# Performance work log

Hardware: AMD Instinct MI355X
Metric: run time of the kernel (lower is better)

## Reference

```python
import jax, jax.numpy as jnp
import numpy as np

B, N, C = 256, 256, 128   # batch (=N_res rows), seq len, pair channels
H, D = 4, 128             # heads, per-head dim (== output_dim per module code)
O = 128                   # output_dim


def _glorot(key, shape, fan_in, fan_out):
    limit = np.sqrt(6.0 / (fan_in + fan_out))
    return jax.random.uniform(key, shape, jnp.float32, -limit, limit)


def setup_inputs() -> dict:
    key = jax.random.key(0)
    ks = jax.random.split(key, 9)
    q_data = jax.random.normal(ks[0], (B, N, C), jnp.float32)
    m_data = jax.random.normal(ks[1], (B, N, C), jnp.float32)
    bias = jax.random.normal(ks[2], (B, 1, N, N), jnp.float32)
    nonbatched_bias = jax.random.normal(ks[3], (H, N, N), jnp.float32)
    query_w = _glorot(ks[4], (C, H, D), C, H * D)
    key_w = _glorot(ks[5], (C, H, D), C, H * D)
    value_w = _glorot(ks[6], (C, H, D), C, H * D)
    gating_w = jnp.zeros((C, H, D), jnp.float32)
    gating_b = jnp.ones((H, D), jnp.float32)
    output_w = _glorot(ks[7], (H, D, O), H * D, O)
    output_b = jnp.zeros((O,), jnp.float32)
    return {
        'q_data': q_data, 'm_data': m_data, 'bias': bias,
        'nonbatched_bias': nonbatched_bias,
        'query_w': query_w, 'key_w': key_w, 'value_w': value_w,
        'gating_w': gating_w, 'gating_b': gating_b,
        'output_w': output_w, 'output_b': output_b,
    }


def reference(q_data, m_data, bias, nonbatched_bias,
              query_w, key_w, value_w, gating_w, gating_b,
              output_w, output_b):
    key_dim = query_w.shape[-1]  # per-head dim (tied to output_dim in module)
    q = jnp.einsum('bqa,ahc->bqhc', q_data, query_w) * key_dim ** (-0.5)
    k = jnp.einsum('bka,ahc->bkhc', m_data, key_w)
    v = jnp.einsum('bka,ahc->bkhc', m_data, value_w)
    logits = jnp.einsum('bqhc,bkhc->bhqk', q, k) + bias
    logits = logits + nonbatched_bias[None]  # broadcast shared bias over batch
    weights = jax.nn.softmax(logits, axis=-1)
    weighted_avg = jnp.einsum('bhqk,bkhc->bqhc', weights, v)
    gate = jax.nn.sigmoid(jnp.einsum('bqc,chv->bqhv', q_data, gating_w) + gating_b)
    weighted_avg = weighted_avg * gate
    return jnp.einsum('bqhc,hco->bqo', weighted_avg, output_w) + output_b
```

## Files before the change

kernel.cpp:

```cpp
#include <hip/hip_runtime.h>
#include <stdint.h>


typedef unsigned short u16;
typedef u16 u16x8 __attribute__((ext_vector_type(8)));
typedef u16 u16x4 __attribute__((ext_vector_type(4)));
typedef __bf16 bf16x8 __attribute__((ext_vector_type(8)));
typedef float floatx4 __attribute__((ext_vector_type(4)));

union B8 { u16x8 u; bf16x8 b; };

__device__ __forceinline__ float bf2f(u16 u) {
  union { uint32_t i; float f; } v; v.i = ((uint32_t)u) << 16; return v.f;
}
__device__ __forceinline__ u16 f2bf(float f) {
  union { float f; uint32_t i; } v; v.f = f;
  return (u16)((v.i + 0x7fffu + ((v.i >> 16) & 1u)) >> 16);
}
__device__ __forceinline__ bf16x8 ld8(const u16* p) { return *(const bf16x8*)p; }
__device__ __forceinline__ floatx4 mfma16(bf16x8 a, bf16x8 b, floatx4 c) {
  return __builtin_amdgcn_mfma_f32_16x16x32_bf16(a, b, c, 0, 0, 0);
}
__device__ __forceinline__ void cfence() { asm volatile("" ::: "memory"); }

template<bool BF>
__device__ __forceinline__ bf16x8 ldin8(const void* p, long long idx) {
  if constexpr (BF) {
    return *(const bf16x8*)((const u16*)p + idx);
  } else {
    const float* f = (const float*)p + idx;
    floatx4 a = *(const floatx4*)f;
    floatx4 b = *(const floatx4*)(f + 4);
    B8 r;
    #pragma unroll
    for (int i = 0; i < 4; ++i) { r.u[i] = f2bf(a[i]); r.u[i + 4] = f2bf(b[i]); }
    return r.b;
  }
}
template<bool BF>
__device__ __forceinline__ float ldin1(const void* p, long long idx) {
  if constexpr (BF) return bf2f(((const u16*)p)[idx]);
  else              return ((const float*)p)[idx];
}

template<bool BF>
__device__ __forceinline__ void pre_body(
    const void* qw, const void* kw, const void* vw, const void* gw,
    const void* ow, u16* wt)
{
  const int blk = blockIdx.x, tid = threadIdx.x;
  if (blk < 16) {
    const int mat = blk >> 2, h = blk & 3;
    const void* W = (mat == 0) ? qw : (mat == 1) ? kw : (mat == 2) ? vw : gw;
    u16* dst = wt + blk * 16384;
    for (int idx = tid; idx < 16384; idx += 256) {
      int c = idx >> 7, d = idx & 127;
      dst[d * 128 + c] = f2bf(ldin1<BF>(W, (long long)c * 512 + h * 128 + d));
    }
  } else {
    const int part = blk - 16;
    u16* dst = wt + 16 * 16384;
    for (int idx = tid; idx < 16384; idx += 256) {
      int k = idx >> 7, o = idx & 127;
      int kg = part * 128 + k;
      dst[o * 512 + kg] = f2bf(ldin1<BF>(ow, (long long)kg * 128 + o));
    }
  }
}

__global__ __launch_bounds__(256) void k_pre(
    const void* qw, const void* kw, const void* vw, const void* gw,
    const void* ow, const void* gating_b, u16* wt)
{
  const bool bf = (*(const uint32_t*)gating_b) == 0x3F803F80u;
  if (bf) pre_body<true >(qw, kw, vw, gw, ow, wt);
  else    pre_body<false>(qw, kw, vw, gw, ow, wt);
}

template<bool BF>
__device__ __forceinline__ void fused_body(
    const void* q_data, const void* m_data,
    const void* __restrict__ bias, const void* __restrict__ nbias,
    const void* gating_b, const u16* __restrict__ wt,
    u16* Ob, int b0, int Bc, u16* smem)
{
  const int tid  = threadIdx.x;
  const int lane = tid & 63, w = tid >> 6;
  const int quad = lane >> 4, l15 = lane & 15;
  const int l7   = l15 & 7;

  const int nwg = Bc * 4, id = blockIdx.x;
  const int xcd = id & 7, rest = id >> 3;
  const int qq = nwg >> 3, rm = nwg & 7;
  const int swz = (xcd < rm ? xcd * (qq + 1) : rm * (qq + 1) + (xcd - rm) * qq) + rest;
  const int bl = swz >> 2, h = swz & 3;
  const int bg = b0 + bl;
  const long long bh = (long long)(bl * 4 + h);

  u16* Kl  = smem;
  u16* Vtl = Kl + 32768;
  u16* sPw = Vtl + 32768 + w * 1152;

  const u16* wtQ = wt + (0 * 4 + h) * 16384;
  const u16* wtK = wt + (1 * 4 + h) * 16384;
  const u16* wtV = wt + (2 * 4 + h) * 16384;
  const u16* wtG = wt + (3 * 4 + h) * 16384;
  const float scale = 0.088388347648318447f;

  bf16x8 aq[2][4];
  u16* Qs = Kl + w * 4096;
  #pragma unroll
  for (int p = 0; p < 2; ++p) {
    const int m0 = p * 128 + w * 16;
    floatx4 qa[8];
    #pragma unroll
    for (int ni = 0; ni < 8; ++ni) qa[ni] = (floatx4){0.f, 0.f, 0.f, 0.f};
    #pragma unroll
    for (int ks = 0; ks < 4; ++ks) {
      bf16x8 aA = ldin8<BF>(q_data, ((long long)bg * 256 + m0 + l15) * 128 + ks * 32 + quad * 8);
      #pragma unroll
      for (int ni = 0; ni < 8; ++ni) {
        bf16x8 bw = ld8(wtQ + (ni * 16 + l15) * 128 + ks * 32 + quad * 8);
        qa[ni] = mfma16(aA, bw, qa[ni]);
      }
    }
    #pragma unroll
    for (int ni = 0; ni < 8; ++ni)
      #pragma unroll
      for (int r = 0; r < 4; ++r)
        Qs[(quad * 4 + r) * 136 + ni * 16 + l15] = f2bf(qa[ni][r] * scale);
    cfence();
    #pragma unroll
    for (int ks = 0; ks < 4; ++ks)
      aq[p][ks] = ld8(Qs + l15 * 136 + ks * 32 + quad * 8);
    cfence();
  }
  __syncthreads();

  const int nb = w * 32;
  {
    floatx4 ka[2][8];
    #pragma unroll
    for (int mi = 0; mi < 2; ++mi)
      #pragma unroll
      for (int ni = 0; ni < 8; ++ni) ka[mi][ni] = (floatx4){0.f, 0.f, 0.f, 0.f};
    #pragma unroll
    for (int ks = 0; ks < 4; ++ks) {
      bf16x8 bw[8];
      #pragma unroll
      for (int ni = 0; ni < 8; ++ni)
        bw[ni] = ld8(wtK + (ni * 16 + l15) * 128 + ks * 32 + quad * 8);
      #pragma unroll
      for (int mi = 0; mi < 2; ++mi) {
        bf16x8 aA = ldin8<BF>(m_data, ((long long)bg * 256 + nb + mi * 16 + l15) * 128 + ks * 32 + quad * 8);
        #pragma unroll
        for (int ni = 0; ni < 8; ++ni)
          ka[mi][ni] = mfma16(aA, bw[ni], ka[mi][ni]);
      }
    }
    #pragma unroll
    for (int mi = 0; mi < 2; ++mi)
      #pragma unroll
      for (int ni = 0; ni < 8; ++ni)
        #pragma unroll
        for (int r = 0; r < 4; ++r) {
          int n = nb + mi * 16 + quad * 4 + r;
          int d = ni * 16 + l15;
          Kl[n * 128 + (d ^ ((n & 7) << 3))] = f2bf(ka[mi][ni][r]);
        }
  }
  {
    floatx4 va[2][8];
    #pragma unroll
    for (int mi = 0; mi < 2; ++mi)
      #pragma unroll
      for (int ni = 0; ni < 8; ++ni) va[mi][ni] = (floatx4){0.f, 0.f, 0.f, 0.f};
    #pragma unroll
    for (int ks = 0; ks < 4; ++ks) {
      bf16x8 bw[8];
      #pragma unroll
      for (int ni = 0; ni < 8; ++ni)
        bw[ni] = ld8(wtV + (ni * 16 + l15) * 128 + ks * 32 + quad * 8);
      #pragma unroll
      for (int mi = 0; mi < 2; ++mi) {
        bf16x8 aA = ldin8<BF>(m_data, ((long long)bg * 256 + nb + mi * 16 + l15) * 128 + ks * 32 + quad * 8);
        #pragma unroll
        for (int ni = 0; ni < 8; ++ni)
          va[mi][ni] = mfma16(aA, bw[ni], va[mi][ni]);
      }
    }
    #pragma unroll
    for (int mi = 0; mi < 2; ++mi)
      #pragma unroll
      for (int ni = 0; ni < 8; ++ni) {
        int d = ni * 16 + l15;
        int n4 = nb + mi * 16 + quad * 4;
        u16x4 v4;
        #pragma unroll
        for (int r = 0; r < 4; ++r) v4[r] = f2bf(va[mi][ni][r]);
        *(u16x4*)(Vtl + d * 256 + (n4 ^ ((d & 7) << 3))) = v4;
      }
  }
  __syncthreads();

  #pragma unroll
  for (int p = 0; p < 2; ++p) {
    const int m0 = p * 128 + w * 16;

    floatx4 s[16];
    #pragma unroll
    for (int nt = 0; nt < 16; ++nt) s[nt] = (floatx4){0.f, 0.f, 0.f, 0.f};
    #pragma unroll
    for (int kc = 0; kc < 4; ++kc) {
      float bz[4][4];
      #pragma unroll
      for (int ntl = 0; ntl < 4; ++ntl)
        #pragma unroll
        for (int r = 0; r < 4; ++r) {
          long long gi = ((long long)bg * 256 + m0 + quad * 4 + r) * 256 + kc * 64 + ntl * 16 + l15;
          long long gn = ((long long)h * 256 + m0 + quad * 4 + r) * 256 + kc * 64 + ntl * 16 + l15;
          bz[ntl][r] = ldin1<BF>(bias, gi) + ldin1<BF>(nbias, gn);
        }
      #pragma unroll
      for (int ntl = 0; ntl < 4; ++ntl) {
        const int nt = kc * 4 + ntl;
        #pragma unroll
        for (int ks = 0; ks < 4; ++ks) {
          bf16x8 bk = ld8(Kl + (kc * 64 + ntl * 16 + l15) * 128 +
                          ((ks * 32 + quad * 8) ^ (l7 << 3)));
          s[nt] = mfma16(aq[p][ks], bk, s[nt]);
        }
        #pragma unroll
        for (int r = 0; r < 4; ++r) s[nt][r] += bz[ntl][r];
      }
    }

    float mx[4] = {-1e30f, -1e30f, -1e30f, -1e30f};
    #pragma unroll
    for (int nt = 0; nt < 16; ++nt)
      #pragma unroll
      for (int r = 0; r < 4; ++r) mx[r] = fmaxf(mx[r], s[nt][r]);
    #pragma unroll
    for (int r = 0; r < 4; ++r)
      #pragma unroll
      for (int off = 1; off < 16; off <<= 1)
        mx[r] = fmaxf(mx[r], __shfl_xor(mx[r], off));
    float sm[4] = {0.f, 0.f, 0.f, 0.f};
    #pragma unroll
    for (int nt = 0; nt < 16; ++nt)
      #pragma unroll
      for (int r = 0; r < 4; ++r) {
        float e = __expf(s[nt][r] - mx[r]);
        s[nt][r] = e; sm[r] += e;
      }
    #pragma unroll
    for (int r = 0; r < 4; ++r)
      #pragma unroll
      for (int off = 1; off < 16; off <<= 1)
        sm[r] += __shfl_xor(sm[r], off);
    float inv[4];
    #pragma unroll
    for (int r = 0; r < 4; ++r) inv[r] = 1.f / sm[r];

    floatx4 o[8];
    #pragma unroll
    for (int dt = 0; dt < 8; ++dt) o[dt] = (floatx4){0.f, 0.f, 0.f, 0.f};
    #pragma unroll
    for (int c = 0; c < 4; ++c) {
      #pragma unroll
      for (int ntl = 0; ntl < 4; ++ntl)
        #pragma unroll
        for (int r = 0; r < 4; ++r)
          sPw[(quad * 4 + r) * 72 + ntl * 16 + l15] = f2bf(s[c * 4 + ntl][r]);
      cfence();
      bf16x8 ap[2];
      #pragma unroll
      for (int k2 = 0; k2 < 2; ++k2)
        ap[k2] = ld8(sPw + l15 * 72 + k2 * 32 + quad * 8);
      #pragma unroll
      for (int dt = 0; dt < 8; ++dt)
        #pragma unroll
        for (int k2 = 0; k2 < 2; ++k2) {
          bf16x8 bv = ld8(Vtl + (dt * 16 + l15) * 256 +
                          ((c * 64 + k2 * 32 + quad * 8) ^ (l7 << 3)));
          o[dt] = mfma16(ap[k2], bv, o[dt]);
        }
      cfence();
    }

    bf16x8 aqd[4];
    #pragma unroll
    for (int ks = 0; ks < 4; ++ks)
      aqd[ks] = ldin8<BF>(q_data, ((long long)bg * 256 + m0 + l15) * 128 + ks * 32 + quad * 8);
    #pragma unroll
    for (int nt = 0; nt < 8; ++nt) {
      floatx4 g = (floatx4){0.f, 0.f, 0.f, 0.f};
      #pragma unroll
      for (int ks = 0; ks < 4; ++ks) {
        bf16x8 bw = ld8(wtG + (nt * 16 + l15) * 128 + ks * 32 + quad * 8);
        g = mfma16(aqd[ks], bw, g);
      }
      #pragma unroll
      for (int r = 0; r < 4; ++r) {
        int row = m0 + quad * 4 + r, d = nt * 16 + l15;
        float gate = 1.f / (1.f + __expf(-(g[r] + ldin1<BF>(gating_b, h * 128 + d))));
        Ob[(bh * 256 + row) * 128 + d] = f2bf(o[nt][r] * inv[r] * gate);
      }
    }
  }
}

__global__ __launch_bounds__(512, 2) void k_fused(
    const void* q_data, const void* m_data, const void* bias,
    const void* nbias, const void* gating_b, const u16* wt,
    u16* Ob, int b0, int Bc)
{
  __shared__ __align__(16) u16 smem[74752];
  const bool bf = (*(const uint32_t*)gating_b) == 0x3F803F80u;
  if (bf) fused_body<true >(q_data, m_data, bias, nbias, gating_b, wt, Ob, b0, Bc, smem);
  else    fused_body<false>(q_data, m_data, bias, nbias, gating_b, wt, Ob, b0, Bc, smem);
}

template<bool BF>
__device__ __forceinline__ void out_body(
    const u16* wsr, const u16* wtO, const void* output_b,
    void* out, int b0)
{
  const int tid  = threadIdx.x;
  const int lane = tid & 63, w = tid >> 6;
  const int quad = lane >> 4, l15 = lane & 15;
  const int wm = w >> 1, wn = w & 1;
  const int r0l = blockIdx.x * 32;
  const int bl  = r0l >> 8, n0 = r0l & 255;

  floatx4 acc[4];
  #pragma unroll
  for (int ni = 0; ni < 4; ++ni) acc[ni] = (floatx4){0.f, 0.f, 0.f, 0.f};

  #pragma unroll
  for (int kt = 0; kt < 4; ++kt) {
    #pragma unroll
    for (int ks = 0; ks < 4; ++ks) {
      bf16x8 af = ld8(wsr + ((long long)(bl * 4 + kt) * 256 + n0 + wm * 16 + l15) * 128
                          + ks * 32 + quad * 8);
      #pragma unroll
      for (int ni = 0; ni < 4; ++ni) {
        int col = wn * 64 + ni * 16 + l15;
        bf16x8 bw = ld8(wtO + (long long)col * 512 + kt * 128 + ks * 32 + quad * 8);
        acc[ni] = mfma16(af, bw, acc[ni]);
      }
    }
  }

  #pragma unroll
  for (int ni = 0; ni < 4; ++ni) {
    #pragma unroll
    for (int r = 0; r < 4; ++r) {
      int i = wm * 16 + quad * 4 + r;
      int j = wn * 64 + ni * 16 + l15;
      long long orow = (long long)b0 * 256 + r0l + i;
      float v = acc[ni][r] + ldin1<BF>(output_b, j);
      if constexpr (BF) ((u16*)out)[orow * 128 + j] = f2bf(v);
      else              ((float*)out)[orow * 128 + j] = v;
    }
  }
}

__global__ __launch_bounds__(256) void k_out(
    const u16* wsr, const u16* wtO, const void* output_b,
    const void* gating_b, void* out, int b0)
{
  const bool bf = (*(const uint32_t*)gating_b) == 0x3F803F80u;
  if (bf) out_body<true >(wsr, wtO, output_b, out, b0);
  else    out_body<false>(wsr, wtO, output_b, out, b0);
}

extern "C" void kernel_launch(void* const* d_in, const int* in_sizes, int n_in,
                              void* d_out, int out_size, void* d_ws, size_t ws_size,
                              hipStream_t stream)
{
  (void)in_sizes; (void)n_in; (void)out_size;
  const void* q_data   = d_in[0];
  const void* m_data   = d_in[1];
  const void* bias     = d_in[2];
  const void* nbias    = d_in[3];
  const void* query_w  = d_in[4];
  const void* key_w    = d_in[5];
  const void* value_w  = d_in[6];
  const void* gating_w = d_in[7];
  const void* gating_b = d_in[8];
  const void* output_w = d_in[9];
  const void* output_b = d_in[10];
  u16* ws = (u16*)d_ws;

  const long long wtElems = 16 * 16384 + 128 * 512;
  u16* wt  = ws;
  u16* wtO = wt + 16 * 16384;
  u16* reg = ws + wtElems;

  const size_t per_batch_bytes = 131072ull * 2;
  const size_t fixed_bytes = (size_t)wtElems * 2;
  int Bc = 1;
  while (Bc * 2 <= 256 &&
         fixed_bytes + (size_t)(Bc * 2) * per_batch_bytes <= ws_size) Bc *= 2;

  k_pre<<<20, 256, 0, stream>>>(query_w, key_w, value_w, gating_w,
                                output_w, gating_b, wt);

  for (int b0 = 0; b0 < 256; b0 += Bc) {
    k_fused<<<Bc * 4, 512, 0, stream>>>(q_data, m_data, bias, nbias,
                                        gating_b, wt, reg, b0, Bc);
    k_out<<<8 * Bc, 256, 0, stream>>>(reg, wtO, output_b,
                                      gating_b, d_out, b0);
  }
}
```

Before: 673.4 us.

## Use 1024-thread blocks with one 16-row query tile per wave, transposed score MFMA

Doubles the fused attention block to 16 waves so each wave handles a single 16-row query tile instead of looping over two. The score MFMA is transposed (K as the A operand), which lets bias and nonbatched bias be read as vectorized 4-wide loads and reduces softmax row reductions to two cross-lane shuffles. P is staged through a swizzled LDS buffer that reuses the K region after a barrier. The trade is fewer registers per thread, an extra block-wide sync, and likely one block per CU.

After: 625.1 us. 1.08x faster.

```diff
diff --git a/kernel.cpp b/kernel.cpp
--- a/kernel.cpp
+++ b/kernel.cpp
@@ -42,6 +42,18 @@
   if constexpr (BF) return bf2f(((const u16*)p)[idx]);
   else              return ((const float*)p)[idx];
 }
+template<bool BF>
+__device__ __forceinline__ floatx4 ldin4(const void* p, long long idx) {
+  floatx4 v;
+  if constexpr (BF) {
+    u16x4 u = *(const u16x4*)((const u16*)p + idx);
+    #pragma unroll
+    for (int i = 0; i < 4; ++i) v[i] = bf2f(u[i]);
+  } else {
+    v = *(const floatx4*)((const float*)p + idx);
+  }
+  return v;
+}
 
 template<bool BF>
 __device__ __forceinline__ void pre_body(
@@ -98,8 +110,7 @@
   const long long bh = (long long)(bl * 4 + h);
 
   u16* Kl  = smem;
-  u16* Vtl = Kl + 32768;
-  u16* sPw = Vtl + 32768 + w * 1152;
+  u16* Vtl = smem + 32768;
 
   const u16* wtQ = wt + (0 * 4 + h) * 16384;
   const u16* wtK = wt + (1 * 4 + h) * 16384;
@@ -107,11 +118,11 @@
   const u16* wtG = wt + (3 * 4 + h) * 16384;
   const float scale = 0.088388347648318447f;
 
-  bf16x8 aq[2][4];
-  u16* Qs = Kl + w * 4096;
-  #pragma unroll
-  for (int p = 0; p < 2; ++p) {
-    const int m0 = p * 128 + w * 16;
+  const int m0 = w * 16;
+
+  bf16x8 aq[4];
+  {
+    u16* Qs = (w < 8) ? (Kl + w * 2176) : (Vtl + (w - 8) * 2176);
     floatx4 qa[8];
     #pragma unroll
     for (int ni = 0; ni < 8; ++ni) qa[ni] = (floatx4){0.f, 0.f, 0.f, 0.f};
@@ -132,190 +143,156 @@
     cfence();
     #pragma unroll
     for (int ks = 0; ks < 4; ++ks)
-      aq[p][ks] = ld8(Qs + l15 * 136 + ks * 32 + quad * 8);
+      aq[ks] = ld8(Qs + l15 * 136 + ks * 32 + quad * 8);
+  }
+  __syncthreads();
+
+  {
+    bf16x8 aA[4];
+    #pragma unroll
+    for (int ks = 0; ks < 4; ++ks)
+      aA[ks] = ldin8<BF>(m_data, ((long long)bg * 256 + m0 + l15) * 128 + ks * 32 + quad * 8);
+
+    floatx4 ka[8];
+    #pragma unroll
+    for (int ni = 0; ni < 8; ++ni) ka[ni] = (floatx4){0.f, 0.f, 0.f, 0.f};
+    #pragma unroll
+    for (int ks = 0; ks < 4; ++ks)
+      #pragma unroll
+      for (int ni = 0; ni < 8; ++ni) {
+        bf16x8 bw = ld8(wtK + (ni * 16 + l15) * 128 + ks * 32 + quad * 8);
+        ka[ni] = mfma16(aA[ks], bw, ka[ni]);
+      }
+    #pragma unroll
+    for (int ni = 0; ni < 8; ++ni)
+      #pragma unroll
+      for (int r = 0; r < 4; ++r) {
+        int n = m0 + quad * 4 + r, d = ni * 16 + l15;
+        Kl[n * 128 + (d ^ ((n & 7) << 3))] = f2bf(ka[ni][r]);
+      }
+
+    floatx4 va[8];
+    #pragma unroll
+    for (int ni = 0; ni < 8; ++ni) va[ni] = (floatx4){0.f, 0.f, 0.f, 0.f};
+    #pragma unroll
+    for (int ks = 0; ks < 4; ++ks)
+      #pragma unroll
+      for (int ni = 0; ni < 8; ++ni) {
+        bf16x8 bw = ld8(wtV + (ni * 16 + l15) * 128 + ks * 32 + quad * 8);
+        va[ni] = mfma16(aA[ks], bw, va[ni]);
+      }
+    #pragma unroll
+    for (int ni = 0; ni < 8; ++ni) {
+      int d = ni * 16 + l15, n4 = m0 + quad * 4;
+      u16x4 vv;
+      #pragma unroll
+      for (int r = 0; r < 4; ++r) vv[r] = f2bf(va[ni][r]);
+      *(u16x4*)(Vtl + d * 256 + (n4 ^ ((d & 7) << 3))) = vv;
+    }
+  }
+  __syncthreads();
+
+  floatx4 s[16];
+  #pragma unroll
+  for (int nt = 0; nt < 16; ++nt) {
+    long long gi = ((long long)bg * 256 + m0 + l15) * 256 + nt * 16 + quad * 4;
+    long long gn = ((long long)h  * 256 + m0 + l15) * 256 + nt * 16 + quad * 4;
+    floatx4 bv = ldin4<BF>(bias, gi);
+    floatx4 nv = ldin4<BF>(nbias, gn);
+    #pragma unroll
+    for (int r = 0; r < 4; ++r) s[nt][r] = bv[r] + nv[r];
+  }
+  #pragma unroll
+  for (int nt = 0; nt < 16; ++nt) {
+    #pragma unroll
+    for (int ks = 0; ks < 4; ++ks) {
+      bf16x8 kf = ld8(Kl + (nt * 16 + l15) * 128 + ((ks * 32 + quad * 8) ^ (l7 << 3)));
+      s[nt] = mfma16(kf, aq[ks], s[nt]);
+    }
+  }
+
+  floatx4 m4 = s[0];
+  #pragma unroll
+  for (int nt = 1; nt < 16; ++nt)
+    #pragma unroll
+    for (int r = 0; r < 4; ++r) m4[r] = fmaxf(m4[r], s[nt][r]);
+  float mx = fmaxf(fmaxf(m4[0], m4[1]), fmaxf(m4[2], m4[3]));
+  mx = fmaxf(mx, __shfl_xor(mx, 16));
+  mx = fmaxf(mx, __shfl_xor(mx, 32));
+
+  u16x4 pk[16];
+  floatx4 s4 = (floatx4){0.f, 0.f, 0.f, 0.f};
+  #pragma unroll
+  for (int nt = 0; nt < 16; ++nt) {
+    #pragma unroll
+    for (int r = 0; r < 4; ++r) {
+      float e = __expf(s[nt][r] - mx);
+      s4[r] += e;
+      pk[nt][r] = f2bf(e);
+    }
+  }
+  float sm = s4[0] + s4[1] + s4[2] + s4[3];
+  sm += __shfl_xor(sm, 16);
+  sm += __shfl_xor(sm, 32);
+  const float inv = 1.f / sm;
+
+  __syncthreads();
+
+  u16* Ps = Kl + w * 2048;
+  floatx4 o[8];
+  #pragma unroll
+  for (int dt = 0; dt < 8; ++dt) o[dt] = (floatx4){0.f, 0.f, 0.f, 0.f};
+  #pragma unroll
+  for (int kh = 0; kh < 2; ++kh) {
+    #pragma unroll
+    for (int nt2 = 0; nt2 < 8; ++nt2)
+      *(u16x4*)(Ps + l15 * 128 + ((nt2 * 16 + quad * 4) ^ (l7 << 3))) = pk[kh * 8 + nt2];
     cfence();
-  }
-  __syncthreads();
-
-  const int nb = w * 32;
-  {
-    floatx4 ka[2][8];
-    #pragma unroll
-    for (int mi = 0; mi < 2; ++mi)
-      #pragma unroll
-      for (int ni = 0; ni < 8; ++ni) ka[mi][ni] = (floatx4){0.f, 0.f, 0.f, 0.f};
+    bf16x8 ap[4];
+    #pragma unroll
+    for (int ks = 0; ks < 4; ++ks)
+      ap[ks] = ld8(Ps + l15 * 128 + ((ks * 32 + quad * 8) ^ (l7 << 3)));
+    #pragma unroll
+    for (int dt = 0; dt < 8; ++dt)
+      #pragma unroll
+      for (int ks = 0; ks < 4; ++ks) {
+        bf16x8 bv = ld8(Vtl + (dt * 16 + l15) * 256 +
+                        ((kh * 128 + ks * 32 + quad * 8) ^ (l7 << 3)));
+        o[dt] = mfma16(ap[ks], bv, o[dt]);
+      }
+    cfence();
+  }
+
+  float invq[4];
+  #pragma unroll
+  for (int r = 0; r < 4; ++r) invq[r] = __shfl(inv, quad * 4 + r);
+  bf16x8 aqd[4];
+  #pragma unroll
+  for (int ks = 0; ks < 4; ++ks)
+    aqd[ks] = ldin8<BF>(q_data, ((long long)bg * 256 + m0 + l15) * 128 + ks * 32 + quad * 8);
+  #pragma unroll
+  for (int nt = 0; nt < 8; ++nt) {
+    floatx4 g = (floatx4){0.f, 0.f, 0.f, 0.f};
     #pragma unroll
     for (int ks = 0; ks < 4; ++ks) {
-      bf16x8 bw[8];
-      #pragma unroll
-      for (int ni = 0; ni < 8; ++ni)
-        bw[ni] = ld8(wtK + (ni * 16 + l15) * 128 + ks * 32 + quad * 8);
-      #pragma unroll
-      for (int mi = 0; mi < 2; ++mi) {
-        bf16x8 aA = ldin8<BF>(m_data, ((long long)bg * 256 + nb + mi * 16 + l15) * 128 + ks * 32 + quad * 8);
-        #pragma unroll
-        for (int ni = 0; ni < 8; ++ni)
-          ka[mi][ni] = mfma16(aA, bw[ni], ka[mi][ni]);
-      }
-    }
-    #pragma unroll
-    for (int mi = 0; mi < 2; ++mi)
-      #pragma unroll
-      for (int ni = 0; ni < 8; ++ni)
-        #pragma unroll
-        for (int r = 0; r < 4; ++r) {
-          int n = nb + mi * 16 + quad * 4 + r;
-          int d = ni * 16 + l15;
-          Kl[n * 128 + (d ^ ((n & 7) << 3))] = f2bf(ka[mi][ni][r]);
-        }
-  }
-  {
-    floatx4 va[2][8];
-    #pragma unroll
-    for (int mi = 0; mi < 2; ++mi)
-      #pragma unroll
-      for (int ni = 0; ni < 8; ++ni) va[mi][ni] = (floatx4){0.f, 0.f, 0.f, 0.f};
-    #pragma unroll
-    for (int ks = 0; ks < 4; ++ks) {
-      bf16x8 bw[8];
-      #pragma unroll
-      for (int ni = 0; ni < 8; ++ni)
-        bw[ni] = ld8(wtV + (ni * 16 + l15) * 128 + ks * 32 + quad * 8);
-      #pragma unroll
-      for (int mi = 0; mi < 2; ++mi) {
-        bf16x8 aA = ldin8<BF>(m_data, ((long long)bg * 256 + nb + mi * 16 + l15) * 128 + ks * 32 + quad * 8);
-        #pragma unroll
-        for (int ni = 0; ni < 8; ++ni)
-          va[mi][ni] = mfma16(aA, bw[ni], va[mi][ni]);
-      }
-    }
-    #pragma unroll
-    for (int mi = 0; mi < 2; ++mi)
-      #pragma unroll
-      for (int ni = 0; ni < 8; ++ni) {
-        int d = ni * 16 + l15;
-        int n4 = nb + mi * 16 + quad * 4;
-        u16x4 v4;
-        #pragma unroll
-        for (int r = 0; r < 4; ++r) v4[r] = f2bf(va[mi][ni][r]);
-        *(u16x4*)(Vtl + d * 256 + (n4 ^ ((d & 7) << 3))) = v4;
-      }
-  }
-  __syncthreads();
-
-  #pragma unroll
-  for (int p = 0; p < 2; ++p) {
-    const int m0 = p * 128 + w * 16;
-
-    floatx4 s[16];
-    #pragma unroll
-    for (int nt = 0; nt < 16; ++nt) s[nt] = (floatx4){0.f, 0.f, 0.f, 0.f};
-    #pragma unroll
-    for (int kc = 0; kc < 4; ++kc) {
-      float bz[4][4];
-      #pragma unroll
-      for (int ntl = 0; ntl < 4; ++ntl)
-        #pragma unroll
-        for (int r = 0; r < 4; ++r) {
-          long long gi = ((long long)bg * 256 + m0 + quad * 4 + r) * 256 + kc * 64 + ntl * 16 + l15;
-          long long gn = ((long long)h * 256 + m0 + quad * 4 + r) * 256 + kc * 64 + ntl * 16 + l15;
-          bz[ntl][r] = ldin1<BF>(bias, gi) + ldin1<BF>(nbias, gn);
-        }
-      #pragma unroll
-      for (int ntl = 0; ntl < 4; ++ntl) {
-        const int nt = kc * 4 + ntl;
-        #pragma unroll
-        for (int ks = 0; ks < 4; ++ks) {
-          bf16x8 bk = ld8(Kl + (kc * 64 + ntl * 16 + l15) * 128 +
-                          ((ks * 32 + quad * 8) ^ (l7 << 3)));
-          s[nt] = mfma16(aq[p][ks], bk, s[nt]);
-        }
-        #pragma unroll
-        for (int r = 0; r < 4; ++r) s[nt][r] += bz[ntl][r];
-      }
-    }
-
-    float mx[4] = {-1e30f, -1e30f, -1e30f, -1e30f};
-    #pragma unroll
-    for (int nt = 0; nt < 16; ++nt)
-      #pragma unroll
-      for (int r = 0; r < 4; ++r) mx[r] = fmaxf(mx[r], s[nt][r]);
-    #pragma unroll
-    for (int r = 0; r < 4; ++r)
-      #pragma unroll
-      for (int off = 1; off < 16; off <<= 1)
-        mx[r] = fmaxf(mx[r], __shfl_xor(mx[r], off));
-    float sm[4] = {0.f, 0.f, 0.f, 0.f};
-    #pragma unroll
-    for (int nt = 0; nt < 16; ++nt)
-      #pragma unroll
-      for (int r = 0; r < 4; ++r) {
-        float e = __expf(s[nt][r] - mx[r]);
-        s[nt][r] = e; sm[r] += e;
-      }
-    #pragma unroll
-    for (int r = 0; r < 4; ++r)
-      #pragma unroll
-      for (int off = 1; off < 16; off <<= 1)
-        sm[r] += __shfl_xor(sm[r], off);
-    float inv[4];
-    #pragma unroll
-    for (int r = 0; r < 4; ++r) inv[r] = 1.f / sm[r];
-
-    floatx4 o[8];
-    #pragma unroll
-    for (int dt = 0; dt < 8; ++dt) o[dt] = (floatx4){0.f, 0.f, 0.f, 0.f};
-    #pragma unroll
-    for (int c = 0; c < 4; ++c) {
-      #pragma unroll
-      for (int ntl = 0; ntl < 4; ++ntl)
-        #pragma unroll
-        for (int r = 0; r < 4; ++r)
-          sPw[(quad * 4 + r) * 72 + ntl * 16 + l15] = f2bf(s[c * 4 + ntl][r]);
-      cfence();
-      bf16x8 ap[2];
-      #pragma unroll
-      for (int k2 = 0; k2 < 2; ++k2)
-        ap[k2] = ld8(sPw + l15 * 72 + k2 * 32 + quad * 8);
-      #pragma unroll
-      for (int dt = 0; dt < 8; ++dt)
-        #pragma unroll
-        for (int k2 = 0; k2 < 2; ++k2) {
-          bf16x8 bv = ld8(Vtl + (dt * 16 + l15) * 256 +
-                          ((c * 64 + k2 * 32 + quad * 8) ^ (l7 << 3)));
-          o[dt] = mfma16(ap[k2], bv, o[dt]);
-        }
-      cfence();
-    }
-
-    bf16x8 aqd[4];
-    #pragma unroll
-    for (int ks = 0; ks < 4; ++ks)
-      aqd[ks] = ldin8<BF>(q_data, ((long long)bg * 256 + m0 + l15) * 128 + ks * 32 + quad * 8);
-    #pragma unroll
-    for (int nt = 0; nt < 8; ++nt) {
-      floatx4 g = (floatx4){0.f, 0.f, 0.f, 0.f};
-      #pragma unroll
-      for (int ks = 0; ks < 4; ++ks) {
-        bf16x8 bw = ld8(wtG + (nt * 16 + l15) * 128 + ks * 32 + quad * 8);
-        g = mfma16(aqd[ks], bw, g);
-      }
-      #pragma unroll
-      for (int r = 0; r < 4; ++r) {
-        int row = m0 + quad * 4 + r, d = nt * 16 + l15;
-        float gate = 1.f / (1.f + __expf(-(g[r] + ldin1<BF>(gating_b, h * 128 + d))));
-        Ob[(bh * 256 + row) * 128 + d] = f2bf(o[nt][r] * inv[r] * gate);
-      }
-    }
-  }
-}
-
-__global__ __launch_bounds__(512, 2) void k_fused(
+      bf16x8 bw = ld8(wtG + (nt * 16 + l15) * 128 + ks * 32 + quad * 8);
+      g = mfma16(aqd[ks], bw, g);
+    }
+    #pragma unroll
+    for (int r = 0; r < 4; ++r) {
+      int row = m0 + quad * 4 + r, d = nt * 16 + l15;
+      float gate = 1.f / (1.f + __expf(-(g[r] + ldin1<BF>(gating_b, h * 128 + d))));
+      Ob[(bh * 256 + row) * 128 + d] = f2bf(o[nt][r] * invq[r] * gate);
+    }
+  }
+}
+
+__global__ __launch_bounds__(1024) void k_fused(
     const void* q_data, const void* m_data, const void* bias,
     const void* nbias, const void* gating_b, const u16* wt,
     u16* Ob, int b0, int Bc)
 {
-  __shared__ __align__(16) u16 smem[74752];
+  __shared__ __align__(16) u16 smem[65536];
   const bool bf = (*(const uint32_t*)gating_b) == 0x3F803F80u;
   if (bf) fused_body<true >(q_data, m_data, bias, nbias, gating_b, wt, Ob, b0, Bc, smem);
   else    fused_body<false>(q_data, m_data, bias, nbias, gating_b, wt, Ob, b0, Bc, smem);
@@ -408,8 +385,8 @@
                                 output_w, gating_b, wt);
 
   for (int b0 = 0; b0 < 256; b0 += Bc) {
-    k_fused<<<Bc * 4, 512, 0, stream>>>(q_data, m_data, bias, nbias,
-                                        gating_b, wt, reg, b0, Bc);
+    k_fused<<<Bc * 4, 1024, 0, stream>>>(q_data, m_data, bias, nbias,
+                                         gating_b, wt, reg, b0, Bc);
     k_out<<<8 * Bc, 256, 0, stream>>>(reg, wtO, output_b,
                                       gating_b, d_out, b0);
   }
```
